# Kernel tuning notes

Hardware: AMD Instinct MI355X
Metric: run time of the kernel (lower is better)

The kernel has to match this reference:

```python
import jax, jax.numpy as jnp
import numpy as np

EMA_BETA = 0.9
NUM_HEADS = 16

def causal_prefix_ema(x, beta):
    # x: [b, t, d]; s_t = beta*s_{t-1} + (1-beta)*x_t, s_{-1}=0
    def step(s, xt):
        s = beta * s + (1.0 - beta) * xt
        return s, s
    s0 = jnp.zeros_like(x[:, 0, :])
    _, ys = jax.lax.scan(step, s0, jnp.swapaxes(x, 0, 1))  # [t, b, d]
    return jnp.swapaxes(ys, 0, 1)

def setup_inputs() -> dict:
    key = jax.random.key(0)
    ks = jax.random.split(key, 9)
    b, t, d = 2, 1024, 2048
    sc = lambda fan_in: 1.0 / np.sqrt(fan_in)
    return {
        "x": jax.random.normal(ks[0], (b, t, d), jnp.float32),
        "l3_memory": jax.random.normal(ks[1], (b, 1, d), jnp.float32),
        "wq": jax.random.normal(ks[2], (d, d), jnp.float32) * sc(d),
        "wk": jax.random.normal(ks[3], (d, d), jnp.float32) * sc(d),
        "wv": jax.random.normal(ks[4], (d, d), jnp.float32) * sc(d),
        "wo": jax.random.normal(ks[5], (d, d), jnp.float32) * sc(d),
        "rw1": jax.random.normal(ks[6], (d // 2, d), jnp.float32) * sc(d),
        "rb1": jnp.zeros((d // 2,), jnp.float32),
        "rw2": jax.random.normal(ks[7], (3, d // 2), jnp.float32) * sc(d // 2),
        "rb2": jnp.zeros((3,), jnp.float32),
    }

def reference(x, l3_memory, wq, wk, wv, wo, rw1, rb1, rw2, rb2):
    b, t, d = x.shape
    h = NUM_HEADS
    dh = d // h
    scale = 1.0 / np.sqrt(dh)

    q = x @ wq.T                                   # [b,t,d]
    l1 = x
    l2 = causal_prefix_ema(x, EMA_BETA)            # [b,t,d]
    l3 = jnp.broadcast_to(l3_memory, (b, t, d))    # repeat retrieval memory to length t

    # router: MLP(Q) -> softmax over 3 levels
    hdn = jax.nn.silu(q @ rw1.T + rb1)
    lam = jax.nn.softmax(hdn @ rw2.T + rb2, axis=-1)  # [b,t,3]

    fused = lam[..., 0:1] * l1 + lam[..., 1:2] * l2 + lam[..., 2:3] * l3

    def heads(y):
        return jnp.swapaxes(y.reshape(b, t, h, dh), 1, 2)  # [b,h,t,dh]

    qh = heads(q)
    kh = heads(fused @ wk.T)
    vh = heads(fused @ wv.T)

    scores = jnp.einsum("bhqd,bhkd->bhqk", qh, kh) * scale
    causal = jnp.tril(jnp.ones((t, t), bool))
    scores = jnp.where(causal, scores, jnp.finfo(scores.dtype).min)
    attn = jax.nn.softmax(scores, axis=-1)
    out = jnp.einsum("bhqk,bhkd->bhqd", attn, vh)

    out = jnp.swapaxes(out, 1, 2).reshape(b, t, d) @ wo.T
    return (out, kh, vh, lam)
```

## Files before the change

### kernel.cpp

```cpp
#include <hip/hip_runtime.h>
#include <hip/hip_bf16.h>
#include <math.h>

#define B_  2
#define T_  1024
#define D_  2048
#define H_  16
#define DH_ 128
#define M_  2048
#define DR_ 1024
#define CH_  16
#define NCH_ 64

typedef __attribute__((ext_vector_type(8))) short short8;
typedef __attribute__((ext_vector_type(4))) short sh4;
typedef __attribute__((ext_vector_type(4))) float f32x4;

__device__ __forceinline__ void gld16(const __hip_bfloat16* g, __hip_bfloat16* l) {
  __builtin_amdgcn_global_load_lds(
      (const __attribute__((address_space(1))) unsigned int*)g,
      (__attribute__((address_space(3))) unsigned int*)l, 16, 0, 0);
}

template<int BM, int CMODE, bool SILU>
__global__ __launch_bounds__(256)
void gemm_mfma(const __hip_bfloat16* __restrict__ A,
               const __hip_bfloat16* __restrict__ Bm,
               const float* __restrict__ bias,
               float* __restrict__ C, __hip_bfloat16* __restrict__ Cb,
               float* __restrict__ C2, __hip_bfloat16* __restrict__ Cb2,
               int M, int N, int K)
{
  constexpr int NI = BM / 32;
  constexpr int AC = BM / 64;
  __shared__ __hip_bfloat16 As[2][2][BM * 32];
  __shared__ __hip_bfloat16 Bs[2][2][128 * 32];
  const int tid  = threadIdx.x;
  const int wave = tid >> 6;
  const int lane = tid & 63;

  const int gx = gridDim.x, gy = gridDim.y;
  const int nwg = gx * gy;
  int lb = blockIdx.y * gx + blockIdx.x;
  lb = (lb & 7) * (nwg >> 3) + (lb >> 3);
  const int ly = __popc(gy - 1);
  const int by = lb & (gy - 1);
  const int bx = lb >> ly;

  const int m0 = by * BM;
  const int n0 = bx * 128;
  const int wm = (wave >> 1) * (BM / 2);
  const int wn = (wave & 1) * 64;

  const int srow = lane >> 2;
  const int scol = (lane & 3) * 8;
  const __hip_bfloat16* Ag = A  + (size_t)(m0 + wave * (BM / 4) + srow) * K + scol;
  const __hip_bfloat16* Bg = Bm + (size_t)(n0 + wave * 32 + srow) * K + scol;

  const int fr = lane & 15;
  const int fk = (lane >> 4) * 8;

  f32x4 acc[NI][4];
  #pragma unroll
  for (int i = 0; i < NI; ++i)
    #pragma unroll
    for (int j = 0; j < 4; ++j) acc[i][j] = (f32x4)0.f;

  auto stage = [&](int bf, int k0) {
    #pragma unroll
    for (int h = 0; h < 2; ++h) {
      #pragma unroll
      for (int c = 0; c < AC; ++c)
        gld16(Ag + k0 + h * 32 + (size_t)(c * 16) * K,
              &As[bf][h][(wave * (BM / 4) + c * 16) * 32]);
      #pragma unroll
      for (int c = 0; c < 2; ++c)
        gld16(Bg + k0 + h * 32 + (size_t)(c * 16) * K,
              &Bs[bf][h][(wave * 32 + c * 16) * 32]);
    }
  };

  stage(0, 0);
  __syncthreads();
  int cur = 0;
  for (int k0 = 0; k0 < K; k0 += 64) {
    if (k0 + 64 < K) stage(cur ^ 1, k0 + 64);
    #pragma unroll
    for (int h = 0; h < 2; ++h) {
      short8 af[NI], bfr[4];
      #pragma unroll
      for (int i = 0; i < NI; ++i)
        af[i]  = *(const short8*)&As[cur][h][(wm + i * 16 + fr) * 32 + fk];
      #pragma unroll
      for (int j = 0; j < 4; ++j)
        bfr[j] = *(const short8*)&Bs[cur][h][(wn + j * 16 + fr) * 32 + fk];
      #pragma unroll
      for (int i = 0; i < NI; ++i)
        #pragma unroll
        for (int j = 0; j < 4; ++j)
          acc[i][j] = __builtin_amdgcn_mfma_f32_16x16x32_bf16(af[i], bfr[j], acc[i][j], 0, 0, 0);
    }
    __syncthreads();
    cur ^= 1;
  }

  #pragma unroll
  for (int i = 0; i < NI; ++i) {
    #pragma unroll
    for (int j = 0; j < 4; ++j) {
      const int row0 = m0 + wm + i * 16 + (lane >> 4) * 4;
      const int col  = n0 + wn + j * 16 + (lane & 15);
      float vr[4];
      #pragma unroll
      for (int r = 0; r < 4; ++r) {
        float v = acc[i][j][r];
        if (bias) v += bias[col];
        if (SILU) v = v / (1.f + __expf(-v));
        vr[r] = v;
      }
      if (CMODE == 0) {
        #pragma unroll
        for (int r = 0; r < 4; ++r) C[(size_t)(row0 + r) * N + col] = vr[r];
      } else if (CMODE == 1) {
        #pragma unroll
        for (int r = 0; r < 4; ++r) Cb[(size_t)(row0 + r) * N + col] = __float2bfloat16(vr[r]);
      } else {
        const int bb = row0 >> 10, t0v = row0 & 1023;
        if (col < D_) {
          const int hh = col >> 7, dd = col & 127;
          #pragma unroll
          for (int r = 0; r < 4; ++r) {
            const size_t idx = (((size_t)(bb * H_ + hh)) * T_ + t0v + r) * DH_ + dd;
            C[idx] = vr[r];
            Cb[idx] = __float2bfloat16(vr[r]);
          }
        } else {
          const int c2 = col - D_;
          const int hh = c2 >> 7, dd = c2 & 127;
          #pragma unroll
          for (int r = 0; r < 4; ++r)
            C2[(((size_t)(bb * H_ + hh)) * T_ + t0v + r) * DH_ + dd] = vr[r];
          __hip_bfloat16 tmp[4];
          #pragma unroll
          for (int r = 0; r < 4; ++r) tmp[r] = __float2bfloat16(vr[r]);
          *(sh4*)(Cb2 + (((size_t)(bb * H_ + hh)) * DH_ + dd) * T_ + t0v) = *(const sh4*)tmp;
        }
      }
    }
  }
}

__global__ __launch_bounds__(256)
void prep_all(const float* __restrict__ x, __hip_bfloat16* __restrict__ xb,
              float* __restrict__ l2, float* __restrict__ lf,
              const float* __restrict__ s1, const float* __restrict__ s2,
              const float* __restrict__ s3, const float* __restrict__ s4,
              const float* __restrict__ s5,
              __hip_bfloat16* d1, __hip_bfloat16* d2, __hip_bfloat16* d3,
              __hip_bfloat16* d4, __hip_bfloat16* d5,
              int n1, int n2, int n3, int n4, int n5)
{
  if (blockIdx.y == 0) {
    const int bid = blockIdx.x;
    if (bid >= 256) return;
    const int dblk = bid & 1;
    const int ch   = (bid >> 1) & 63;
    const int b    = bid >> 7;
    const int t0 = ch * CH_;
    const int d  = dblk * 1024 + threadIdx.x * 4;
    const float* xp = x  + (size_t)b * T_ * D_ + d;
    float*       lp = l2 + (size_t)b * T_ * D_ + d;
    __hip_bfloat16* xo = xb + (size_t)b * T_ * D_ + d;
    float4 s = make_float4(0.f, 0.f, 0.f, 0.f);
    #pragma unroll 4
    for (int t = t0; t < t0 + CH_; ++t) {
      float4 v = *(const float4*)(xp + (size_t)t * D_);
      __hip_bfloat16 tmp[4] = {__float2bfloat16(v.x), __float2bfloat16(v.y),
                               __float2bfloat16(v.z), __float2bfloat16(v.w)};
      *(sh4*)(xo + (size_t)t * D_) = *(const sh4*)tmp;
      s.x = 0.9f * s.x + 0.1f * v.x;
      s.y = 0.9f * s.y + 0.1f * v.y;
      s.z = 0.9f * s.z + 0.1f * v.z;
      s.w = 0.9f * s.w + 0.1f * v.w;
      *(float4*)(lp + (size_t)t * D_) = s;
    }
    *(float4*)(lf + ((size_t)b * NCH_ + ch) * D_ + d) = s;
    return;
  }
  const float* s; __hip_bfloat16* d; int n;
  switch (blockIdx.y) {
    case 1: s = s1; d = d1; n = n1; break;
    case 2: s = s2; d = d2; n = n2; break;
    case 3: s = s3; d = d3; n = n3; break;
    case 4: s = s4; d = d4; n = n4; break;
    default: s = s5; d = d5; n = n5; break;
  }
  const int i = (blockIdx.x * 256 + threadIdx.x) * 8;
  if (i < n) {
    float4 a = *(const float4*)(s + i);
    float4 b = *(const float4*)(s + i + 4);
    __hip_bfloat16 t[8] = {__float2bfloat16(a.x), __float2bfloat16(a.y),
                           __float2bfloat16(a.z), __float2bfloat16(a.w),
                           __float2bfloat16(b.x), __float2bfloat16(b.y),
                           __float2bfloat16(b.z), __float2bfloat16(b.w)};
    *(short8*)(d + i) = *(const short8*)t;
  }
}

__global__ __launch_bounds__(256)
void fuse_router(const float* __restrict__ x, const float* __restrict__ l2,
                 const float* __restrict__ l3m, const float* __restrict__ hdn,
                 const float* __restrict__ rw2, const float* __restrict__ rb2,
                 const float* __restrict__ lf, float* __restrict__ lam,
                 __hip_bfloat16* __restrict__ fb)
{
  __shared__ float lamS[8][3];
  const int tid = threadIdx.x;
  const int g = tid >> 5, l32 = tid & 31;
  const int m = blockIdx.x * 8 + g;
  const float* hp = hdn + (size_t)m * DR_;
  float s0 = 0.f, s1 = 0.f, s2 = 0.f;
  #pragma unroll
  for (int it = 0; it < 8; ++it) {
    const int k = l32 * 4 + it * 128;
    float4 h4 = *(const float4*)(hp + k);
    float4 w0 = *(const float4*)(rw2 + k);
    float4 w1 = *(const float4*)(rw2 + DR_ + k);
    float4 w2 = *(const float4*)(rw2 + 2 * DR_ + k);
    s0 += h4.x * w0.x + h4.y * w0.y + h4.z * w0.z + h4.w * w0.w;
    s1 += h4.x * w1.x + h4.y * w1.y + h4.z * w1.z + h4.w * w1.w;
    s2 += h4.x * w2.x + h4.y * w2.y + h4.z * w2.z + h4.w * w2.w;
  }
  #pragma unroll
  for (int off = 16; off > 0; off >>= 1) {
    s0 += __shfl_xor(s0, off);
    s1 += __shfl_xor(s1, off);
    s2 += __shfl_xor(s2, off);
  }
  if (l32 == 0) {
    s0 += rb2[0]; s1 += rb2[1]; s2 += rb2[2];
    float mx = fmaxf(s0, fmaxf(s1, s2));
    float e0 = __expf(s0 - mx), e1 = __expf(s1 - mx), e2 = __expf(s2 - mx);
    float inv = 1.f / (e0 + e1 + e2);
    lam[(size_t)m * 3 + 0] = e0 * inv;
    lam[(size_t)m * 3 + 1] = e1 * inv;
    lam[(size_t)m * 3 + 2] = e2 * inv;
    lamS[g][0] = e0 * inv; lamS[g][1] = e1 * inv; lamS[g][2] = e2 * inv;
  }

  const int m0b = blockIdx.x * 8;
  const int bb  = m0b >> 10;
  const int ch  = (m0b & 1023) >> 4;
  const int c   = tid * 8;
  float4 cv0 = make_float4(0.f, 0.f, 0.f, 0.f);
  float4 cv1 = make_float4(0.f, 0.f, 0.f, 0.f);
  {
    float w = 1.f;
    for (int j = ch - 1; j >= 0; --j) {
      const float* lp = lf + ((size_t)bb * NCH_ + j) * D_ + c;
      float4 a0 = *(const float4*)(lp);
      float4 a1 = *(const float4*)(lp + 4);
      cv0.x += w * a0.x; cv0.y += w * a0.y; cv0.z += w * a0.z; cv0.w += w * a0.w;
      cv1.x += w * a1.x; cv1.y += w * a1.y; cv1.z += w * a1.z; cv1.w += w * a1.w;
      w *= 0.18530201888518416f;
    }
  }
  __syncthreads();

  const int base = m0b & 15;
  #pragma unroll
  for (int r = 0; r < 8; ++r) {
    const int mm = m0b + r;
    const float pw = __expf((float)(base + r + 1) * -0.105360515657f);
    const float u0 = lamS[r][0], u1 = lamS[r][1], u2 = lamS[r][2];
    const float* xp = x   + (size_t)mm * D_ + c;
    const float* ep = l2  + (size_t)mm * D_ + c;
    const float* gp = l3m + (size_t)bb * D_ + c;
    __hip_bfloat16 tmp[8];
    {
      float4 xv = *(const float4*)(xp);
      float4 ev = *(const float4*)(ep);
      float4 gv = *(const float4*)(gp);
      tmp[0] = __float2bfloat16(u0 * xv.x + u1 * (ev.x + pw * cv0.x) + u2 * gv.x);
      tmp[1] = __float2bfloat16(u0 * xv.y + u1 * (ev.y + pw * cv0.y) + u2 * gv.y);
      tmp[2] = __float2bfloat16(u0 * xv.z + u1 * (ev.z + pw * cv0.z) + u2 * gv.z);
      tmp[3] = __float2bfloat16(u0 * xv.w + u1 * (ev.w + pw * cv0.w) + u2 * gv.w);
    }
    {
      float4 xv = *(const float4*)(xp + 4);
      float4 ev = *(const float4*)(ep + 4);
      float4 gv = *(const float4*)(gp + 4);
      tmp[4] = __float2bfloat16(u0 * xv.x + u1 * (ev.x + pw * cv1.x) + u2 * gv.x);
      tmp[5] = __float2bfloat16(u0 * xv.y + u1 * (ev.y + pw * cv1.y) + u2 * gv.y);
      tmp[6] = __float2bfloat16(u0 * xv.z + u1 * (ev.z + pw * cv1.z) + u2 * gv.z);
      tmp[7] = __float2bfloat16(u0 * xv.w + u1 * (ev.w + pw * cv1.w) + u2 * gv.w);
    }
    *(short8*)(fb + (size_t)mm * D_ + c) = *(const short8*)tmp;
  }
}

__global__ __launch_bounds__(256)
void flash_mfma(const __hip_bfloat16* __restrict__ qg,
                const __hip_bfloat16* __restrict__ kg,
                const __hip_bfloat16* __restrict__ vg,
                __hip_bfloat16* __restrict__ og)
{
  __shared__ __hip_bfloat16 Ks[2][64 * 136];
  __shared__ __hip_bfloat16 Vt[2][128 * 72];
  __shared__ __hip_bfloat16 Ps[64 * 72];
  const int tid  = threadIdx.x;
  const int wave = tid >> 6, lane = tid & 63;
  const int L    = blockIdx.x;
  const int halfg = L >> 8, idx = L & 255;
  const int bh = (idx >> 4) | (halfg << 4);
  const int qt = halfg ? (15 - (idx & 15)) : (idx & 15);
  const int b = bh >> 4, h = bh & 15;
  const int q0 = qt * 64;
  const int lo = lane & 15, hi = lane >> 4;

  short8 aq[4];
  {
    const __hip_bfloat16* qsrc = qg + (size_t)(b * T_ + q0 + wave * 16 + lo) * D_ + h * DH_;
    #pragma unroll
    for (int kk = 0; kk < 4; ++kk)
      aq[kk] = *(const short8*)(qsrc + kk * 32 + hi * 8);
  }

  f32x4 oacc[8];
  #pragma unroll
  for (int i = 0; i < 8; ++i) oacc[i] = (f32x4)0.f;
  float mrow[4] = {-INFINITY, -INFINITY, -INFINITY, -INFINITY};
  float lrow[4] = {0.f, 0.f, 0.f, 0.f};

  const __hip_bfloat16* kbp = kg + (size_t)bh * T_ * DH_;
  const __hip_bfloat16* vbp = vg + (size_t)bh * DH_ * T_;
  const float scale = 0.08838834764831845f;

  short8 kreg[4], vreg[4];
  auto load_tile = [&](int k0) {
    #pragma unroll
    for (int i = 0; i < 4; ++i) {
      const int ci = tid + 256 * i;
      const int r = ci >> 4, j = ci & 15;
      kreg[i] = *(const short8*)(kbp + (size_t)(k0 + r) * DH_ + j * 8);
      const int dd = ci >> 3, j2 = ci & 7;
      vreg[i] = *(const short8*)(vbp + (size_t)dd * T_ + k0 + j2 * 8);
    }
  };
  auto write_lds = [&](int bf) {
    #pragma unroll
    for (int i = 0; i < 4; ++i) {
      const int ci = tid + 256 * i;
      const int r = ci >> 4, j = ci & 15;
      *(short8*)&Ks[bf][r * 136 + j * 8] = kreg[i];
      const int dd = ci >> 3, j2 = ci & 7;
      *(short8*)&Vt[bf][dd * 72 + j2 * 8] = vreg[i];
    }
  };

  load_tile(0);
  write_lds(0);
  if (qt > 0) load_tile(64);
  __syncthreads();

  for (int kt = 0; kt <= qt; ++kt) {
    const int cur = kt & 1;
    f32x4 sc[4];
    __builtin_amdgcn_s_setprio(1);
    #pragma unroll
    for (int nt = 0; nt < 4; ++nt) {
      sc[nt] = (f32x4)0.f;
      #pragma unroll
      for (int kk = 0; kk < 4; ++kk) {
        short8 bk = *(const short8*)&Ks[cur][(nt * 16 + lo) * 136 + kk * 32 + hi * 8];
        sc[nt] = __builtin_amdgcn_mfma_f32_16x16x32_bf16(aq[kk], bk, sc[nt], 0, 0, 0);
      }
    }
    __builtin_amdgcn_s_setprio(0);
    #pragma unroll
    for (int nt = 0; nt < 4; ++nt)
      #pragma unroll
      for (int r = 0; r < 4; ++r) sc[nt][r] *= scale;
    if (kt == qt) {
      const int qrow = q0 + wave * 16 + hi * 4;
      #pragma unroll
      for (int nt = 0; nt < 4; ++nt) {
        const int key = qt * 64 + nt * 16 + lo;
        #pragma unroll
        for (int r = 0; r < 4; ++r)
          if (key > qrow + r) sc[nt][r] = -1e30f;
      }
    }
    float alpha[4];
    #pragma unroll
    for (int r = 0; r < 4; ++r) {
      float mx = fmaxf(fmaxf(sc[0][r], sc[1][r]), fmaxf(sc[2][r], sc[3][r]));
      mx = fmaxf(mx, __shfl_xor(mx, 1));
      mx = fmaxf(mx, __shfl_xor(mx, 2));
      mx = fmaxf(mx, __shfl_xor(mx, 4));
      mx = fmaxf(mx, __shfl_xor(mx, 8));
      const float nm = fmaxf(mrow[r], mx);
      alpha[r] = __expf(mrow[r] - nm);
      mrow[r] = nm;
      float ls = 0.f;
      #pragma unroll
      for (int nt = 0; nt < 4; ++nt) {
        float p = __expf(sc[nt][r] - nm);
        sc[nt][r] = p;
        ls += p;
      }
      ls += __shfl_xor(ls, 1);
      ls += __shfl_xor(ls, 2);
      ls += __shfl_xor(ls, 4);
      ls += __shfl_xor(ls, 8);
      lrow[r] = lrow[r] * alpha[r] + ls;
    }
    #pragma unroll
    for (int nt = 0; nt < 4; ++nt)
      #pragma unroll
      for (int r = 0; r < 4; ++r)
        Ps[(wave * 16 + hi * 4 + r) * 72 + nt * 16 + lo] = __float2bfloat16(sc[nt][r]);
    #pragma unroll
    for (int n2 = 0; n2 < 8; ++n2)
      #pragma unroll
      for (int r = 0; r < 4; ++r) oacc[n2][r] *= alpha[r];
    short8 ap[2];
    #pragma unroll
    for (int k2 = 0; k2 < 2; ++k2)
      ap[k2] = *(const short8*)&Ps[(wave * 16 + lo) * 72 + k2 * 32 + hi * 8];
    __builtin_amdgcn_s_setprio(1);
    #pragma unroll
    for (int n2 = 0; n2 < 8; ++n2) {
      #pragma unroll
      for (int k2 = 0; k2 < 2; ++k2) {
        short8 bv = *(const short8*)&Vt[cur][(n2 * 16 + lo) * 72 + k2 * 32 + hi * 8];
        oacc[n2] = __builtin_amdgcn_mfma_f32_16x16x32_bf16(ap[k2], bv, oacc[n2], 0, 0, 0);
      }
    }
    __builtin_amdgcn_s_setprio(0);
    if (kt < qt) {
      write_lds(cur ^ 1);
      if (kt + 1 < qt) load_tile((kt + 2) * 64);
    }
    __syncthreads();
  }

  float inv[4];
  #pragma unroll
  for (int r = 0; r < 4; ++r) inv[r] = 1.f / lrow[r];
  __hip_bfloat16* od = og + (size_t)(b * T_ + q0 + wave * 16 + hi * 4) * D_ + h * DH_;
  #pragma unroll
  for (int n2 = 0; n2 < 8; ++n2)
    #pragma unroll
    for (int r = 0; r < 4; ++r)
      od[(size_t)r * D_ + n2 * 16 + lo] = __float2bfloat16(oacc[n2][r] * inv[r]);
}

extern "C" void kernel_launch(void* const* d_in, const int* in_sizes, int n_in,
                              void* d_out, int out_size, void* d_ws, size_t ws_size,
                              hipStream_t stream)
{
  const float* x   = (const float*)d_in[0];
  const float* l3m = (const float*)d_in[1];
  const float* wq  = (const float*)d_in[2];
  const float* wk  = (const float*)d_in[3];
  const float* wv  = (const float*)d_in[4];
  const float* wo  = (const float*)d_in[5];
  const float* rw1 = (const float*)d_in[6];
  const float* rb1 = (const float*)d_in[7];
  const float* rw2 = (const float*)d_in[8];
  const float* rb2 = (const float*)d_in[9];

  float* out = (float*)d_out;
  float* kh  = out + 4194304;
  float* vh  = out + 8388608;
  float* lam = out + 12582912;

  char* wsb = (char*)d_ws;
  float*          l2_f32 = (float*)(wsb);
  float*          hdn    = (float*)(wsb + (16u << 20));
  __hip_bfloat16* wkb    = (__hip_bfloat16*)(wsb + (24u << 20));
  __hip_bfloat16* wvb    = (__hip_bfloat16*)(wsb + (32u << 20));
  __hip_bfloat16* wob    = (__hip_bfloat16*)(wsb + (40u << 20));
  __hip_bfloat16* fusedb = (__hip_bfloat16*)(wsb + (48u << 20));
  __hip_bfloat16* attnb  = (__hip_bfloat16*)(wsb + (56u << 20));
  __hip_bfloat16* khb    = (__hip_bfloat16*)(wsb + (64u << 20));
  __hip_bfloat16* vtb    = (__hip_bfloat16*)(wsb + (72u << 20));
  float*          lf     = (float*)(wsb + (57u << 20));
  __hip_bfloat16* wqb  = (__hip_bfloat16*)kh;
  __hip_bfloat16* rw1b = (__hip_bfloat16*)kh + 4194304;
  __hip_bfloat16* xb   = (__hip_bfloat16*)vh;
  __hip_bfloat16* qb   = (__hip_bfloat16*)out;

  dim3 blk(256);

  prep_all<<<dim3(2048, 6), blk, 0, stream>>>(x, xb, l2_f32, lf,
                                              wq, wk, wv, wo, rw1,
                                              wqb, wkb, wvb, wob, rw1b,
                                              D_ * D_, D_ * D_, D_ * D_, D_ * D_, DR_ * D_);
  gemm_mfma<64, 1, false><<<dim3(16, 32), blk, 0, stream>>>(xb, wqb, nullptr, nullptr, qb, nullptr, nullptr, M_, D_, D_);
  gemm_mfma<64, 0, true><<<dim3(8, 32), blk, 0, stream>>>(qb, rw1b, rb1, hdn, nullptr, nullptr, nullptr, M_, DR_, D_);
  fuse_router<<<dim3(256), blk, 0, stream>>>(x, l2_f32, l3m, hdn, rw2, rb2, lf, lam, fusedb);
  gemm_mfma<128, 4, false><<<dim3(32, 16), blk, 0, stream>>>(fusedb, wkb, nullptr, kh, khb, vh, vtb, M_, 2 * D_, D_);
  flash_mfma<<<dim3(512), blk, 0, stream>>>(qb, khb, vtb, attnb);
  gemm_mfma<64, 0, false><<<dim3(16, 32), blk, 0, stream>>>(attnb, wob, nullptr, out, nullptr, nullptr, nullptr, M_, D_, D_);
}
```

Baseline: 346.6 us.

## Defer softmax rescaling in flash attention and drop GEMM tile swizzle

The attention kernel now skips the running-max update and accumulator rescale when every lane's new tile max stays within a threshold of the current max, and keeps per-lane partial row sums that are reduced across lanes only once at the end. This removes per-tile shuffles, exp calls and output rescaling in the common case, at the cost of a wave-wide vote and a divergent branch. The GEMM kernel also drops its XCD-aware block-index remapping and uses plain blockIdx order, which may change L2 locality across chiplets.

```diff
diff --git a/kernel.cpp b/kernel.cpp
--- a/kernel.cpp
+++ b/kernel.cpp
@@ -38,17 +38,8 @@
   const int tid  = threadIdx.x;
   const int wave = tid >> 6;
   const int lane = tid & 63;
-
-  const int gx = gridDim.x, gy = gridDim.y;
-  const int nwg = gx * gy;
-  int lb = blockIdx.y * gx + blockIdx.x;
-  lb = (lb & 7) * (nwg >> 3) + (lb >> 3);
-  const int ly = __popc(gy - 1);
-  const int by = lb & (gy - 1);
-  const int bx = lb >> ly;
-
-  const int m0 = by * BM;
-  const int n0 = bx * 128;
+  const int m0 = blockIdx.y * BM;
+  const int n0 = blockIdx.x * 128;
   const int wm = (wave >> 1) * (BM / 2);
   const int wn = (wave & 1) * 64;
 
@@ -329,8 +320,8 @@
   f32x4 oacc[8];
   #pragma unroll
   for (int i = 0; i < 8; ++i) oacc[i] = (f32x4)0.f;
-  float mrow[4] = {-INFINITY, -INFINITY, -INFINITY, -INFINITY};
-  float lrow[4] = {0.f, 0.f, 0.f, 0.f};
+  float mrow[4]  = {-INFINITY, -INFINITY, -INFINITY, -INFINITY};
+  float lrowp[4] = {0.f, 0.f, 0.f, 0.f};
 
   const __hip_bfloat16* kbp = kg + (size_t)bh * T_ * DH_;
   const __hip_bfloat16* vbp = vg + (size_t)bh * DH_ * T_;
@@ -391,7 +382,7 @@
           if (key > qrow + r) sc[nt][r] = -1e30f;
       }
     }
-    float alpha[4];
+    float mxv[4];
     #pragma unroll
     for (int r = 0; r < 4; ++r) {
       float mx = fmaxf(fmaxf(sc[0][r], sc[1][r]), fmaxf(sc[2][r], sc[3][r]));
@@ -399,31 +390,48 @@
       mx = fmaxf(mx, __shfl_xor(mx, 2));
       mx = fmaxf(mx, __shfl_xor(mx, 4));
       mx = fmaxf(mx, __shfl_xor(mx, 8));
-      const float nm = fmaxf(mrow[r], mx);
-      alpha[r] = __expf(mrow[r] - nm);
-      mrow[r] = nm;
-      float ls = 0.f;
-      #pragma unroll
-      for (int nt = 0; nt < 4; ++nt) {
-        float p = __expf(sc[nt][r] - nm);
-        sc[nt][r] = p;
-        ls += p;
-      }
-      ls += __shfl_xor(ls, 1);
-      ls += __shfl_xor(ls, 2);
-      ls += __shfl_xor(ls, 4);
-      ls += __shfl_xor(ls, 8);
-      lrow[r] = lrow[r] * alpha[r] + ls;
+      mxv[r] = mx;
+    }
+    const bool deferLane = (mxv[0] <= mrow[0] + 8.f) & (mxv[1] <= mrow[1] + 8.f) &
+                           (mxv[2] <= mrow[2] + 8.f) & (mxv[3] <= mrow[3] + 8.f);
+    if (__all(deferLane)) {
+      #pragma unroll
+      for (int r = 0; r < 4; ++r) {
+        float ls = 0.f;
+        #pragma unroll
+        for (int nt = 0; nt < 4; ++nt) {
+          float p = __expf(sc[nt][r] - mrow[r]);
+          sc[nt][r] = p;
+          ls += p;
+        }
+        lrowp[r] += ls;
+      }
+    } else {
+      float alpha[4];
+      #pragma unroll
+      for (int r = 0; r < 4; ++r) {
+        const float nm = fmaxf(mrow[r], mxv[r]);
+        alpha[r] = __expf(mrow[r] - nm);
+        mrow[r] = nm;
+        float ls = 0.f;
+        #pragma unroll
+        for (int nt = 0; nt < 4; ++nt) {
+          float p = __expf(sc[nt][r] - nm);
+          sc[nt][r] = p;
+          ls += p;
+        }
+        lrowp[r] = lrowp[r] * alpha[r] + ls;
+      }
+      #pragma unroll
+      for (int n2 = 0; n2 < 8; ++n2)
+        #pragma unroll
+        for (int r = 0; r < 4; ++r) oacc[n2][r] *= alpha[r];
     }
     #pragma unroll
     for (int nt = 0; nt < 4; ++nt)
       #pragma unroll
       for (int r = 0; r < 4; ++r)
         Ps[(wave * 16 + hi * 4 + r) * 72 + nt * 16 + lo] = __float2bfloat16(sc[nt][r]);
-    #pragma unroll
-    for (int n2 = 0; n2 < 8; ++n2)
-      #pragma unroll
-      for (int r = 0; r < 4; ++r) oacc[n2][r] *= alpha[r];
     short8 ap[2];
     #pragma unroll
     for (int k2 = 0; k2 < 2; ++k2)
@@ -447,7 +455,14 @@
 
   float inv[4];
   #pragma unroll
-  for (int r = 0; r < 4; ++r) inv[r] = 1.f / lrow[r];
+  for (int r = 0; r < 4; ++r) {
+    float l = lrowp[r];
+    l += __shfl_xor(l, 1);
+    l += __shfl_xor(l, 2);
+    l += __shfl_xor(l, 4);
+    l += __shfl_xor(l, 8);
+    inv[r] = 1.f / l;
+  }
   __hip_bfloat16* od = og + (size_t)(b * T_ + q0 + wave * 16 + hi * 4) * D_ + h * DH_;
   #pragma unroll
   for (int n2 = 0; n2 < 8; ++n2)
```

Result: no change. 341.2 us (-1.6%).
